# Optimization experiments

Hardware: AMD Instinct MI355X
Metric: run time of the kernel (lower is better)

The kernel has to match this reference:

```python
import jax, jax.numpy as jnp
import numpy as np

N = 8192
H = 256
NF = 256  # number of fragment segments
LOG2 = 0.6931471805599453
R = 0.3        # short_long_ratio
C = 0.8        # brics_consistency_strength
VW = 0.5       # vector_weight


def _ssp(x):
    # ShiftedSoftplus: softplus(x) - log(2)
    return jax.nn.softplus(x) - LOG2


def _l2norm(x):
    # F.normalize(p=2, dim=1) semantics with eps clamp
    n = jnp.linalg.norm(x, axis=1, keepdims=True)
    return x / jnp.maximum(n, 1e-12)


def _pair_sim_err_per_frag(feat, fragment_ids, pair_mask):
    # sum over same-fragment upper-tri pairs of (cos_sim - C)^2, per fragment
    z = _l2norm(feat)                       # [N,H]
    S = z @ z.T                             # [N,N]
    err = jnp.where(pair_mask, (S - C) ** 2, 0.0)
    return jax.ops.segment_sum(err.sum(axis=1), fragment_ids, num_segments=NF)


def setup_inputs() -> dict:
    key = jax.random.key(0)
    ks = jax.random.split(key, 12)
    s = 1.0 / np.sqrt(H)
    return {
        "scalar_short": jax.random.normal(ks[0], (N, H), dtype=jnp.float32),
        "scalar_long": jax.random.normal(ks[1], (N, H), dtype=jnp.float32),
        "vector_short": jax.random.normal(ks[2], (N, 3, H), dtype=jnp.float32),
        "vector_long": jax.random.normal(ks[3], (N, 3, H), dtype=jnp.float32),
        "W1": jax.random.normal(ks[4], (H, H), dtype=jnp.float32) * s,
        "b1": jnp.zeros((H,), dtype=jnp.float32),
        "W2": jax.random.normal(ks[5], (H, H), dtype=jnp.float32) * s,
        "b2": jnp.zeros((H,), dtype=jnp.float32),
        "V1": jax.random.normal(ks[6], (H, H), dtype=jnp.float32) * s,
        "V2": jax.random.normal(ks[7], (H, H), dtype=jnp.float32) * s,
        "fragment_ids": jax.random.randint(ks[8], (N,), 0, NF, dtype=jnp.int64),
    }


def reference(scalar_short, scalar_long, vector_short, vector_long,
              W1, b1, W2, b2, V1, V2, fragment_ids):
    frag = fragment_ids
    counts = jax.ops.segment_sum(jnp.ones((N,), jnp.float32), frag, num_segments=NF)
    n_safe = jnp.maximum(counts, 1.0)
    pair_count = counts * (counts - 1.0) * 0.5
    pc_safe = jnp.maximum(pair_count, 1.0)

    idx = jnp.arange(N)
    # same-fragment, strictly-upper-triangular pair mask [N,N]
    pair_mask = (frag[:, None] == frag[None, :]) & (idx[None, :] > idx[:, None])

    # ---- scalar branch ----
    sc = scalar_short * R + scalar_long * (1.0 - R)
    si = _ssp(sc @ W1 + b1) @ W2 + b2                     # [N,H]
    s_mean = jax.ops.segment_sum(si, frag, num_segments=NF) / n_safe[:, None]
    s_dev = si - s_mean[frag]
    s_var = jax.ops.segment_sum((s_dev ** 2).sum(axis=1), frag, num_segments=NF) / n_safe
    s_sim = _pair_sim_err_per_frag(si, frag, pair_mask) / pc_safe
    scalar_loss = s_var + s_sim

    # ---- vector branch ----
    vc = vector_short * R + vector_long * (1.0 - R)
    vi = _ssp(vc @ V1) @ V2                               # [N,3,H]
    v_mean = jax.ops.segment_sum(vi, frag, num_segments=NF) / n_safe[:, None, None]
    v_dev = vi - v_mean[frag]
    v_var = jax.ops.segment_sum((v_dev ** 2).sum(axis=(1, 2)), frag, num_segments=NF) / n_safe
    dir_err = jnp.zeros((NF,), jnp.float32)
    for d in range(3):
        dir_err = dir_err + _pair_sim_err_per_frag(vi[:, d, :], frag, pair_mask)
    dir_loss = dir_err / (3.0 * pc_safe)
    vector_loss = v_var + dir_loss

    frag_loss = (1.0 - VW) * scalar_loss + VW * vector_loss
    valid = pair_count > 0.0   # fragments with >= 2 nodes
    vcnt = valid.sum().astype(jnp.float32)
    total = jnp.where(valid, frag_loss, 0.0).sum()
    return jnp.where(vcnt > 0.0, total / jnp.maximum(vcnt, 1.0), 0.0)
```

## Files before the change

### kernel.cpp

```cpp
#include <hip/hip_runtime.h>
#include <cmath>

#define N_NODES 8192
#define HDIM 256
#define NFRAG 256
#define RMIX 0.3f
#define CSIM 0.8f
#define LN2 0.6931471805599453f
#define CMAX 64

typedef __bf16 bf16x8 __attribute__((ext_vector_type(8)));
typedef float f32x4 __attribute__((ext_vector_type(4)));
typedef unsigned short us8 __attribute__((ext_vector_type(8)));
typedef unsigned short us4 __attribute__((ext_vector_type(4)));
typedef unsigned short ushort_t;

#define SI_OFF   ((size_t)0)
#define VI_OFF   ((size_t)8388608)
#define WH_OFF   ((size_t)58720256)
#define WL_OFF   ((size_t)59244544)
#define CNT_OFF  ((size_t)59768832)
#define CUR_OFF  (CNT_OFF + 1024)
#define OFF_OFF  (CNT_OFF + 2048)
#define SORT_OFF (CNT_OFF + 3072)
#define ACC_OFF  (SORT_OFF + 32768)
#define FLG_OFF  (ACC_OFF + 128)
#define NRM_OFF  (ACC_OFF + 256)
#define FRGN_OFF (NRM_OFF + 4 * 32768)

__device__ __forceinline__ ushort_t f2bf(float x) {
    unsigned u = __float_as_uint(x);
    return (ushort_t)((u + 0x7FFFu + ((u >> 16) & 1u)) >> 16);
}
__device__ __forceinline__ float bf2f(ushort_t h) {
    return __uint_as_float(((unsigned)h) << 16);
}
__device__ __forceinline__ f32x4 mfma_bf16(us8 a, us8 b, f32x4 c) {
    return __builtin_amdgcn_mfma_f32_16x16x32_bf16(
        __builtin_bit_cast(bf16x8, a), __builtin_bit_cast(bf16x8, b), c, 0, 0, 0);
}


__global__ void init_kernel(int* counts, int* cursor, float* acc, int* flag) {
    int t = threadIdx.x;
    if (t < NFRAG) { counts[t] = 0; cursor[t] = 0; }
    if (t < 8) acc[t] = 0.f;
    if (t == 0) *flag = 0;
}

__global__ void detect_kernel(const int* __restrict__ buf, int* flag) {
    int i = blockIdx.x * 256 + threadIdx.x;
    if (buf[2 * i + 1] != 0) atomicOr(flag, 1);
}

__global__ void normalize_kernel(const int* __restrict__ buf, const int* __restrict__ flag,
                                 int* __restrict__ fragN) {
    int i = blockIdx.x * 256 + threadIdx.x;
    if (i < N_NODES) fragN[i] = (*flag) ? buf[i] : buf[2 * i];
}

__global__ void hist_kernel(const int* __restrict__ frag, int* counts) {
    int i = blockIdx.x * 256 + threadIdx.x;
    if (i < N_NODES) atomicAdd(&counts[frag[i]], 1);
}

__global__ void scan_kernel(const int* __restrict__ counts, int* offs) {
    __shared__ int tmp[NFRAG];
    int t = threadIdx.x;
    tmp[t] = counts[t];
    __syncthreads();
    for (int off = 1; off < NFRAG; off <<= 1) {
        int v = (t >= off) ? tmp[t - off] : 0;
        __syncthreads();
        tmp[t] += v;
        __syncthreads();
    }
    offs[t] = tmp[t] - counts[t];
}

__global__ void scatter_kernel(const int* __restrict__ frag, const int* __restrict__ offs,
                               int* cursor, int* sorted) {
    int i = blockIdx.x * 256 + threadIdx.x;
    if (i < N_NODES) {
        int f = frag[i];
        int pos = offs[f] + atomicAdd(&cursor[f], 1);
        sorted[pos] = i;
    }
}

__global__ void wsplit_kernel(const float* __restrict__ W1, const float* __restrict__ W2,
                              const float* __restrict__ V1, const float* __restrict__ V2,
                              ushort_t* __restrict__ Whi, ushort_t* __restrict__ Wlo) {
    int m = blockIdx.y;
    const float* src = (m == 0) ? W1 : (m == 1) ? W2 : (m == 2) ? V1 : V2;
    ushort_t* dh = Whi + m * 65536;
    ushort_t* dl = Wlo + m * 65536;
    int o = blockIdx.x * 256 + threadIdx.x;
    int e = o & 7, kg = (o >> 3) & 3, n = (o >> 5) & 255, kb = o >> 13;
    float x = src[(size_t)(kb * 32 + kg * 8 + e) * HDIM + n];
    ushort_t h = f2bf(x);
    dh[o] = h;
    dl[o] = f2bf(x - bf2f(h));
}


template<bool BIAS1, bool BIAS2>
__global__ __launch_bounds__(256)
void mlp_fused(const float* __restrict__ A0, const float* __restrict__ A1,
               const ushort_t* __restrict__ B1h, const ushort_t* __restrict__ B1l,
               const ushort_t* __restrict__ B2h, const ushort_t* __restrict__ B2l,
               const float* __restrict__ b1, const float* __restrict__ b2,
               float* __restrict__ Out)
{
    __shared__ ushort_t Zh[32 * 256];
    __shared__ ushort_t Zl[32 * 256];

    const int tid = threadIdx.x;
    const int l   = tid & 63;
    const int wid = tid >> 6;
    const int lr  = l & 15;
    const int kg  = l >> 4;
    const int rowBase = blockIdx.x * 32;
    const int colW = wid * 64;

    {
        int r  = tid >> 3;
        int c0 = (tid & 7) * 32;
        const float* ps = A0 + (size_t)(rowBase + r) * HDIM + c0;
        const float* pl = A1 + (size_t)(rowBase + r) * HDIM + c0;
        int swz = (r & 7) << 3;
        #pragma unroll
        for (int cc = 0; cc < 4; ++cc) {
            float4 s0 = *(const float4*)(ps + cc * 8);
            float4 s1 = *(const float4*)(ps + cc * 8 + 4);
            float4 t0 = *(const float4*)(pl + cc * 8);
            float4 t1 = *(const float4*)(pl + cc * 8 + 4);
            float x[8];
            x[0] = s0.x * RMIX + t0.x * (1.f - RMIX);
            x[1] = s0.y * RMIX + t0.y * (1.f - RMIX);
            x[2] = s0.z * RMIX + t0.z * (1.f - RMIX);
            x[3] = s0.w * RMIX + t0.w * (1.f - RMIX);
            x[4] = s1.x * RMIX + t1.x * (1.f - RMIX);
            x[5] = s1.y * RMIX + t1.y * (1.f - RMIX);
            x[6] = s1.z * RMIX + t1.z * (1.f - RMIX);
            x[7] = s1.w * RMIX + t1.w * (1.f - RMIX);
            us8 h, lo;
            #pragma unroll
            for (int e = 0; e < 8; ++e) {
                ushort_t hh = f2bf(x[e]);
                h[e] = hh;
                lo[e] = f2bf(x[e] - bf2f(hh));
            }
            int idx = r * 256 + ((c0 + cc * 8) ^ swz);
            *(us8*)&Zh[idx] = h;
            *(us8*)&Zl[idx] = lo;
        }
    }
    __syncthreads();

    const ushort_t *w1h[4], *w1l[4], *w2h[4], *w2l[4];
    #pragma unroll
    for (int nf = 0; nf < 4; ++nf) {
        int n = colW + nf * 16 + lr;
        int off = n * 32 + kg * 8;
        w1h[nf] = B1h + off;  w1l[nf] = B1l + off;
        w2h[nf] = B2h + off;  w2l[nf] = B2l + off;
    }

    f32x4 acc[2][4];
    #pragma unroll
    for (int mf = 0; mf < 2; ++mf)
        #pragma unroll
        for (int nf = 0; nf < 4; ++nf)
            acc[mf][nf] = f32x4{0.f, 0.f, 0.f, 0.f};

    for (int kb = 0; kb < 8; ++kb) {
        const int kx = kb * 32 + kg * 8;
        us8 ah[2], al[2];
        #pragma unroll
        for (int mf = 0; mf < 2; ++mf) {
            int m = mf * 16 + lr;
            int idx = m * 256 + (kx ^ ((m & 7) << 3));
            ah[mf] = *(const us8*)&Zh[idx];
            al[mf] = *(const us8*)&Zl[idx];
        }
        #pragma unroll
        for (int nf = 0; nf < 4; ++nf) {
            us8 wh = *(const us8*)(w1h[nf] + kb * 8192);
            us8 wl = *(const us8*)(w1l[nf] + kb * 8192);
            #pragma unroll
            for (int mf = 0; mf < 2; ++mf) {
                f32x4 t = acc[mf][nf];
                t = mfma_bf16(wl, al[mf], t);
                t = mfma_bf16(wl, ah[mf], t);
                t = mfma_bf16(wh, al[mf], t);
                t = mfma_bf16(wh, ah[mf], t);
                acc[mf][nf] = t;
            }
        }
    }
    __syncthreads();

    #pragma unroll
    for (int mf = 0; mf < 2; ++mf) {
        int m = mf * 16 + lr;
        #pragma unroll
        for (int nf = 0; nf < 4; ++nf) {
            int n0 = colW + nf * 16 + kg * 4;
            float4 bb = {0.f, 0.f, 0.f, 0.f};
            if constexpr (BIAS1) bb = *(const float4*)(b1 + n0);
            us4 h4, l4;
            #pragma unroll
            for (int r = 0; r < 4; ++r) {
                float x = acc[mf][nf][r] + ((const float*)&bb)[r];
                x = fmaxf(x, 0.f) + log1pf(__expf(-fabsf(x))) - LN2;
                ushort_t hh = f2bf(x);
                h4[r] = hh;
                l4[r] = f2bf(x - bf2f(hh));
            }
            int idx = m * 256 + (n0 ^ ((m & 7) << 3));
            *(us4*)&Zh[idx] = h4;
            *(us4*)&Zl[idx] = l4;
        }
    }
    __syncthreads();

    f32x4 acc2[2][4];
    #pragma unroll
    for (int mf = 0; mf < 2; ++mf)
        #pragma unroll
        for (int nf = 0; nf < 4; ++nf)
            acc2[mf][nf] = f32x4{0.f, 0.f, 0.f, 0.f};

    for (int kb = 0; kb < 8; ++kb) {
        const int kx = kb * 32 + kg * 8;
        us8 ah[2], al[2];
        #pragma unroll
        for (int mf = 0; mf < 2; ++mf) {
            int m = mf * 16 + lr;
            int idx = m * 256 + (kx ^ ((m & 7) << 3));
            ah[mf] = *(const us8*)&Zh[idx];
            al[mf] = *(const us8*)&Zl[idx];
        }
        #pragma unroll
        for (int nf = 0; nf < 4; ++nf) {
            us8 wh = *(const us8*)(w2h[nf] + kb * 8192);
            us8 wl = *(const us8*)(w2l[nf] + kb * 8192);
            #pragma unroll
            for (int mf = 0; mf < 2; ++mf) {
                f32x4 t = acc2[mf][nf];
                t = mfma_bf16(wl, al[mf], t);
                t = mfma_bf16(wl, ah[mf], t);
                t = mfma_bf16(wh, al[mf], t);
                t = mfma_bf16(wh, ah[mf], t);
                acc2[mf][nf] = t;
            }
        }
    }

    #pragma unroll
    for (int mf = 0; mf < 2; ++mf) {
        int row = rowBase + mf * 16 + lr;
        #pragma unroll
        for (int nf = 0; nf < 4; ++nf) {
            int n0 = colW + nf * 16 + kg * 4;
            float4 bb = {0.f, 0.f, 0.f, 0.f};
            if constexpr (BIAS2) bb = *(const float4*)(b2 + n0);
            float4 v;
            v.x = acc2[mf][nf][0] + bb.x;
            v.y = acc2[mf][nf][1] + bb.y;
            v.z = acc2[mf][nf][2] + bb.z;
            v.w = acc2[mf][nf][3] + bb.w;
            *(float4*)(Out + (size_t)row * HDIM + n0) = v;
        }
    }
}


__device__ __forceinline__ float blockReduceSum(float v, float* red) {
    #pragma unroll
    for (int off = 32; off > 0; off >>= 1)
        v += __shfl_down(v, off, 64);
    __syncthreads();
    if ((threadIdx.x & 63) == 0) red[threadIdx.x >> 6] = v;
    __syncthreads();
    return red[0] + red[1] + red[2] + red[3];
}

__device__ __forceinline__ float dot4(float4 a, float4 b) {
    return a.x * b.x + a.y * b.y + a.z * b.z + a.w * b.w;
}

__device__ void compute_invn_g(const float* __restrict__ Mat, int mult, int doff,
                               int c, int basep, const int* __restrict__ sorted,
                               float* invn, int tid)
{
    for (int p = tid; p < c; p += 256) {
        int nd = sorted[basep + p];
        const float4* row = (const float4*)(Mat + ((size_t)nd * mult + doff) * HDIM);
        float ss = 0.f;
        #pragma unroll 8
        for (int k = 0; k < 64; ++k) {
            float4 v = row[k];
            ss += v.x * v.x + v.y * v.y + v.z * v.z + v.w * v.w;
        }
        invn[p] = 1.0f / fmaxf(sqrtf(ss), 1e-12f);
    }
}

__device__ float pair_err_slow(const float* __restrict__ Mat, int mult, int doff,
                               int c, int basep, const int* __restrict__ sorted,
                               const float* invn, int tid)
{
    float e = 0.f;
    for (long pi = tid; pi < (long)c * c; pi += 256) {
        int i = (int)(pi / c), j = (int)(pi - (long)i * c);
        if (j <= i) continue;
        const float4* ri = (const float4*)(Mat + ((size_t)sorted[basep + i] * mult + doff) * HDIM);
        const float4* rj = (const float4*)(Mat + ((size_t)sorted[basep + j] * mult + doff) * HDIM);
        float dt = 0.f;
        for (int k = 0; k < 64; ++k) dt += dot4(ri[k], rj[k]);
        float sv = dt * invn[i] * invn[j];
        float d = sv - CSIM;
        e += d * d;
    }
    return e;
}

__global__ __launch_bounds__(256)
void fragmat_kernel(const float* __restrict__ SI, const float* __restrict__ VI,
                    const int* __restrict__ counts, const int* __restrict__ offs,
                    const int* __restrict__ sorted, float* acc, float* nrm_global)
{
    const int f = blockIdx.x, m = blockIdx.y, tid = threadIdx.x;
    const int c = counts[f];
    if (c < 2) return;
    const int basep = offs[f];
    const float* Mat = (m == 0) ? SI : VI;
    const int mult = (m == 0) ? 1 : 3;
    const int doff = (m == 0) ? 0 : (m - 1);

    __shared__ __align__(16) float Z[CMAX * 260];
    __shared__ float invn_s[CMAX];
    __shared__ float red[4];

    float var, err;

    if (c <= CMAX) {
        for (int u = tid; u < c * 64; u += 256) {
            int r = u >> 6, kc = u & 63;
            float4 v = *((const float4*)(Mat + ((size_t)sorted[basep + r] * mult + doff) * HDIM) + kc);
            *(float4*)&Z[r * 260 + (kc << 2)] = v;
        }
        __syncthreads();

        float msum = 0.f;
        for (int p = 0; p < c; ++p) msum += Z[p * 260 + tid];
        float mean = msum / (float)c;
        float vh = 0.f;
        for (int p = 0; p < c; ++p) {
            float d = Z[p * 260 + tid] - mean;
            vh += d * d;
        }
        var = blockReduceSum(vh, red);

        for (int p = tid; p < c; p += 256) {
            const float4* row = (const float4*)&Z[p * 260];
            float ss = 0.f;
            #pragma unroll 8
            for (int k = 0; k < 64; ++k) {
                float4 v = row[k];
                ss += v.x * v.x + v.y * v.y + v.z * v.z + v.w * v.w;
            }
            invn_s[p] = 1.0f / fmaxf(sqrtf(ss), 1e-12f);
        }
        __syncthreads();

        const int nb2 = (c + 1) >> 1;
        const int nbp = nb2 * (nb2 + 1) / 2;
        float e = 0.f;
        for (int u = tid; u < nbp; u += 256) {
            int bi = 0, rem = u;
            while (rem >= nb2 - bi) { rem -= nb2 - bi; ++bi; }
            int bj = bi + rem;
            int i0 = bi << 1, j0 = bj << 1;
            const float* zi0 = &Z[i0 * 260];
            const float* zi1 = &Z[(i0 + 1) * 260];
            const float* zj0 = &Z[j0 * 260];
            const float* zj1 = &Z[(j0 + 1) * 260];
            float s00 = 0.f, s01 = 0.f, s10 = 0.f, s11 = 0.f;
            #pragma unroll 4
            for (int k = 0; k < 64; ++k) {
                float4 a0 = *(const float4*)(zi0 + (k << 2));
                float4 a1 = *(const float4*)(zi1 + (k << 2));
                float4 b0 = *(const float4*)(zj0 + (k << 2));
                float4 b1 = *(const float4*)(zj1 + (k << 2));
                s00 += dot4(a0, b0);
                s01 += dot4(a0, b1);
                s10 += dot4(a1, b0);
                s11 += dot4(a1, b1);
            }
            int i1 = i0 + 1, j1 = j0 + 1;
            if (j0 > i0 && j0 < c) { float sv = s00 * invn_s[i0] * invn_s[j0] - CSIM; e += sv * sv; }
            if (j1 > i0 && j1 < c) { float sv = s01 * invn_s[i0] * invn_s[j1] - CSIM; e += sv * sv; }
            if (j0 > i1 && j0 < c) { float sv = s10 * invn_s[i1] * invn_s[j0] - CSIM; e += sv * sv; }
            if (j1 > i1 && j1 < c) { float sv = s11 * invn_s[i1] * invn_s[j1] - CSIM; e += sv * sv; }
        }
        err = blockReduceSum(e, red);
    } else {
        float msum = 0.f;
        for (int p = 0; p < c; ++p)
            msum += Mat[((size_t)sorted[basep + p] * mult + doff) * HDIM + tid];
        float mean = msum / (float)c;
        float vh = 0.f;
        for (int p = 0; p < c; ++p) {
            float d = Mat[((size_t)sorted[basep + p] * mult + doff) * HDIM + tid] - mean;
            vh += d * d;
        }
        var = blockReduceSum(vh, red);

        float* invn = nrm_global + (size_t)m * N_NODES + basep;
        compute_invn_g(Mat, mult, doff, c, basep, sorted, invn, tid);
        __syncthreads();
        float e = pair_err_slow(Mat, mult, doff, c, basep, sorted, invn, tid);
        err = blockReduceSum(e, red);
    }

    if (tid == 0) {
        float n = (float)c;
        float pc = 0.5f * n * (n - 1.f);
        float w_err = (m == 0) ? (0.5f / pc) : (0.5f / (3.f * pc));
        float contrib = 0.5f * var / n + err * w_err;
        atomicAdd(&acc[0], contrib);
        if (m == 0) atomicAdd(&acc[1], 1.0f);
    }
}

__global__ void finalize_kernel(const float* __restrict__ acc, float* __restrict__ out) {
    if (threadIdx.x == 0)
        out[0] = (acc[1] > 0.f) ? acc[0] / acc[1] : 0.f;
}


extern "C" void kernel_launch(void* const* d_in, const int* in_sizes, int n_in,
                              void* d_out, int out_size, void* d_ws, size_t ws_size,
                              hipStream_t stream) {
    const float* s_short = (const float*)d_in[0];
    const float* s_long  = (const float*)d_in[1];
    const float* v_short = (const float*)d_in[2];
    const float* v_long  = (const float*)d_in[3];
    const float* W1 = (const float*)d_in[4];
    const float* b1 = (const float*)d_in[5];
    const float* W2 = (const float*)d_in[6];
    const float* b2 = (const float*)d_in[7];
    const float* V1 = (const float*)d_in[8];
    const float* V2 = (const float*)d_in[9];
    const int* fragRaw = (const int*)d_in[10];
    float* out = (float*)d_out;

    char* ws = (char*)d_ws;
    float*    SI     = (float*)(ws + SI_OFF);
    float*    VI     = (float*)(ws + VI_OFF);
    ushort_t* WH     = (ushort_t*)(ws + WH_OFF);
    ushort_t* WL     = (ushort_t*)(ws + WL_OFF);
    int*      counts = (int*)(ws + CNT_OFF);
    int*      cursor = (int*)(ws + CUR_OFF);
    int*      offs   = (int*)(ws + OFF_OFF);
    int*      sorted = (int*)(ws + SORT_OFF);
    float*    acc    = (float*)(ws + ACC_OFF);
    int*      flag   = (int*)(ws + FLG_OFF);
    float*    nrm    = (float*)(ws + NRM_OFF);
    int*      fragN  = (int*)(ws + FRGN_OFF);

    init_kernel<<<1, 256, 0, stream>>>(counts, cursor, acc, flag);
    detect_kernel<<<16, 256, 0, stream>>>(fragRaw, flag);
    normalize_kernel<<<N_NODES / 256, 256, 0, stream>>>(fragRaw, flag, fragN);
    hist_kernel<<<N_NODES / 256, 256, 0, stream>>>(fragN, counts);
    scan_kernel<<<1, 256, 0, stream>>>(counts, offs);
    scatter_kernel<<<N_NODES / 256, 256, 0, stream>>>(fragN, offs, cursor, sorted);
    wsplit_kernel<<<dim3(256, 4), 256, 0, stream>>>(W1, W2, V1, V2, WH, WL);

    mlp_fused<true, true><<<dim3(N_NODES / 32), 256, 0, stream>>>(
        s_short, s_long, WH + 0 * 65536, WL + 0 * 65536,
        WH + 1 * 65536, WL + 1 * 65536, b1, b2, SI);
    mlp_fused<false, false><<<dim3(3 * N_NODES / 32), 256, 0, stream>>>(
        v_short, v_long, WH + 2 * 65536, WL + 2 * 65536,
        WH + 3 * 65536, WL + 3 * 65536, nullptr, nullptr, VI);

    fragmat_kernel<<<dim3(NFRAG, 4), 256, 0, stream>>>(SI, VI, counts, offs, sorted, acc, nrm);
    finalize_kernel<<<1, 64, 0, stream>>>(acc, out);
}
```

Measured before the change: 255.1 us.

## Merge scalar and vector MLP launches and double row tile to 64

Replaces the two templated MLP launches with one kernel that picks the scalar or vector branch per block from its row index. The block's row tile grows from 32 to 64, so each weight fragment loaded from global memory feeds four M-fragments instead of two, which halves weight traffic per row. The softplus log1pf is also swapped for the faster __logf(1+x). The cost is doubled LDS (64KB) and more accumulator registers, which may lower occupancy, plus a small accuracy change in the softplus.

Measured after the change: 209.5 us. 17.9% less time.

```diff
diff --git a/kernel.cpp b/kernel.cpp
--- a/kernel.cpp
+++ b/kernel.cpp
@@ -104,33 +104,49 @@
 }
 
 
-template<bool BIAS1, bool BIAS2>
 __global__ __launch_bounds__(256)
-void mlp_fused(const float* __restrict__ A0, const float* __restrict__ A1,
-               const ushort_t* __restrict__ B1h, const ushort_t* __restrict__ B1l,
-               const ushort_t* __restrict__ B2h, const ushort_t* __restrict__ B2l,
-               const float* __restrict__ b1, const float* __restrict__ b2,
-               float* __restrict__ Out)
+void mlp_fused_all(const float* __restrict__ s_short, const float* __restrict__ s_long,
+                   const float* __restrict__ v_short, const float* __restrict__ v_long,
+                   const ushort_t* __restrict__ WH, const ushort_t* __restrict__ WL,
+                   const float* __restrict__ b1, const float* __restrict__ b2,
+                   float* __restrict__ SI, float* __restrict__ VI)
 {
-    __shared__ ushort_t Zh[32 * 256];
-    __shared__ ushort_t Zl[32 * 256];
+    __shared__ __align__(16) ushort_t Zh[64 * 256];
+    __shared__ __align__(16) ushort_t Zl[64 * 256];
 
     const int tid = threadIdx.x;
     const int l   = tid & 63;
     const int wid = tid >> 6;
     const int lr  = l & 15;
     const int kg  = l >> 4;
-    const int rowBase = blockIdx.x * 32;
     const int colW = wid * 64;
 
+    const int rowBase = blockIdx.x * 64;
+    const bool isScalar = (rowBase < N_NODES);
+    const float* A0;
+    const float* A1;
+    float* Out;
+    const ushort_t *B1h, *B1l, *B2h, *B2l;
+    if (isScalar) {
+        size_t off = (size_t)rowBase * HDIM;
+        A0 = s_short + off;  A1 = s_long + off;  Out = SI + off;
+        B1h = WH;              B1l = WL;
+        B2h = WH + 65536;      B2l = WL + 65536;
+    } else {
+        size_t off = (size_t)(rowBase - N_NODES) * HDIM;
+        A0 = v_short + off;  A1 = v_long + off;  Out = VI + off;
+        B1h = WH + 2 * 65536;  B1l = WL + 2 * 65536;
+        B2h = WH + 3 * 65536;  B2l = WL + 3 * 65536;
+    }
+
     {
-        int r  = tid >> 3;
-        int c0 = (tid & 7) * 32;
-        const float* ps = A0 + (size_t)(rowBase + r) * HDIM + c0;
-        const float* pl = A1 + (size_t)(rowBase + r) * HDIM + c0;
+        int r  = tid >> 2;
+        int c0 = (tid & 3) * 64;
+        const float* ps = A0 + (size_t)r * HDIM + c0;
+        const float* pl = A1 + (size_t)r * HDIM + c0;
         int swz = (r & 7) << 3;
         #pragma unroll
-        for (int cc = 0; cc < 4; ++cc) {
+        for (int cc = 0; cc < 8; ++cc) {
             float4 s0 = *(const float4*)(ps + cc * 8);
             float4 s1 = *(const float4*)(ps + cc * 8 + 4);
             float4 t0 = *(const float4*)(pl + cc * 8);
@@ -158,62 +174,60 @@
     }
     __syncthreads();
 
-    const ushort_t *w1h[4], *w1l[4], *w2h[4], *w2l[4];
+    const int wbase = (colW + lr) * 32 + kg * 8;
+
+    f32x4 acc[4][4];
     #pragma unroll
-    for (int nf = 0; nf < 4; ++nf) {
-        int n = colW + nf * 16 + lr;
-        int off = n * 32 + kg * 8;
-        w1h[nf] = B1h + off;  w1l[nf] = B1l + off;
-        w2h[nf] = B2h + off;  w2l[nf] = B2l + off;
-    }
-
-    f32x4 acc[2][4];
-    #pragma unroll
-    for (int mf = 0; mf < 2; ++mf)
+    for (int mf = 0; mf < 4; ++mf)
         #pragma unroll
         for (int nf = 0; nf < 4; ++nf)
             acc[mf][nf] = f32x4{0.f, 0.f, 0.f, 0.f};
 
-    for (int kb = 0; kb < 8; ++kb) {
-        const int kx = kb * 32 + kg * 8;
-        us8 ah[2], al[2];
-        #pragma unroll
-        for (int mf = 0; mf < 2; ++mf) {
-            int m = mf * 16 + lr;
-            int idx = m * 256 + (kx ^ ((m & 7) << 3));
-            ah[mf] = *(const us8*)&Zh[idx];
-            al[mf] = *(const us8*)&Zl[idx];
-        }
-        #pragma unroll
-        for (int nf = 0; nf < 4; ++nf) {
-            us8 wh = *(const us8*)(w1h[nf] + kb * 8192);
-            us8 wl = *(const us8*)(w1l[nf] + kb * 8192);
+    {
+        const ushort_t* ph = B1h + wbase;
+        const ushort_t* pl = B1l + wbase;
+        for (int kb = 0; kb < 8; ++kb) {
+            const int kx = kb * 32 + kg * 8;
+            us8 ah[4], al[4];
             #pragma unroll
-            for (int mf = 0; mf < 2; ++mf) {
-                f32x4 t = acc[mf][nf];
-                t = mfma_bf16(wl, al[mf], t);
-                t = mfma_bf16(wl, ah[mf], t);
-                t = mfma_bf16(wh, al[mf], t);
-                t = mfma_bf16(wh, ah[mf], t);
-                acc[mf][nf] = t;
-            }
+            for (int mf = 0; mf < 4; ++mf) {
+                int m = mf * 16 + lr;
+                int idx = m * 256 + (kx ^ ((m & 7) << 3));
+                ah[mf] = *(const us8*)&Zh[idx];
+                al[mf] = *(const us8*)&Zl[idx];
+            }
+            #pragma unroll
+            for (int nf = 0; nf < 4; ++nf) {
+                us8 wh = *(const us8*)(ph + nf * 512);
+                us8 wl = *(const us8*)(pl + nf * 512);
+                #pragma unroll
+                for (int mf = 0; mf < 4; ++mf) {
+                    f32x4 t = acc[mf][nf];
+                    t = mfma_bf16(wl, al[mf], t);
+                    t = mfma_bf16(wl, ah[mf], t);
+                    t = mfma_bf16(wh, al[mf], t);
+                    t = mfma_bf16(wh, ah[mf], t);
+                    acc[mf][nf] = t;
+                }
+            }
+            ph += 8192; pl += 8192;
         }
     }
     __syncthreads();
 
     #pragma unroll
-    for (int mf = 0; mf < 2; ++mf) {
+    for (int mf = 0; mf < 4; ++mf) {
         int m = mf * 16 + lr;
         #pragma unroll
         for (int nf = 0; nf < 4; ++nf) {
             int n0 = colW + nf * 16 + kg * 4;
             float4 bb = {0.f, 0.f, 0.f, 0.f};
-            if constexpr (BIAS1) bb = *(const float4*)(b1 + n0);
+            if (isScalar) bb = *(const float4*)(b1 + n0);
             us4 h4, l4;
             #pragma unroll
             for (int r = 0; r < 4; ++r) {
                 float x = acc[mf][nf][r] + ((const float*)&bb)[r];
-                x = fmaxf(x, 0.f) + log1pf(__expf(-fabsf(x))) - LN2;
+                x = fmaxf(x, 0.f) + __logf(1.f + __expf(-fabsf(x))) - LN2;
                 ushort_t hh = f2bf(x);
                 h4[r] = hh;
                 l4[r] = f2bf(x - bf2f(hh));
@@ -225,53 +239,58 @@
     }
     __syncthreads();
 
-    f32x4 acc2[2][4];
+    f32x4 acc2[4][4];
     #pragma unroll
-    for (int mf = 0; mf < 2; ++mf)
+    for (int mf = 0; mf < 4; ++mf)
         #pragma unroll
         for (int nf = 0; nf < 4; ++nf)
             acc2[mf][nf] = f32x4{0.f, 0.f, 0.f, 0.f};
 
-    for (int kb = 0; kb < 8; ++kb) {
-        const int kx = kb * 32 + kg * 8;
-        us8 ah[2], al[2];
-        #pragma unroll
-        for (int mf = 0; mf < 2; ++mf) {
-            int m = mf * 16 + lr;
-            int idx = m * 256 + (kx ^ ((m & 7) << 3));
-            ah[mf] = *(const us8*)&Zh[idx];
-            al[mf] = *(const us8*)&Zl[idx];
-        }
-        #pragma unroll
-        for (int nf = 0; nf < 4; ++nf) {
-            us8 wh = *(const us8*)(w2h[nf] + kb * 8192);
-            us8 wl = *(const us8*)(w2l[nf] + kb * 8192);
+    {
+        const ushort_t* ph = B2h + wbase;
+        const ushort_t* pl = B2l + wbase;
+        for (int kb = 0; kb < 8; ++kb) {
+            const int kx = kb * 32 + kg * 8;
+            us8 ah[4], al[4];
             #pragma unroll
-            for (int mf = 0; mf < 2; ++mf) {
-                f32x4 t = acc2[mf][nf];
-                t = mfma_bf16(wl, al[mf], t);
-                t = mfma_bf16(wl, ah[mf], t);
-                t = mfma_bf16(wh, al[mf], t);
-                t = mfma_bf16(wh, ah[mf], t);
-                acc2[mf][nf] = t;
-            }
+            for (int mf = 0; mf < 4; ++mf) {
+                int m = mf * 16 + lr;
+                int idx = m * 256 + (kx ^ ((m & 7) << 3));
+                ah[mf] = *(const us8*)&Zh[idx];
+                al[mf] = *(const us8*)&Zl[idx];
+            }
+            #pragma unroll
+            for (int nf = 0; nf < 4; ++nf) {
+                us8 wh = *(const us8*)(ph + nf * 512);
+                us8 wl = *(const us8*)(pl + nf * 512);
+                #pragma unroll
+                for (int mf = 0; mf < 4; ++mf) {
+                    f32x4 t = acc2[mf][nf];
+                    t = mfma_bf16(wl, al[mf], t);
+                    t = mfma_bf16(wl, ah[mf], t);
+                    t = mfma_bf16(wh, al[mf], t);
+                    t = mfma_bf16(wh, ah[mf], t);
+                    acc2[mf][nf] = t;
+                }
+            }
+            ph += 8192; pl += 8192;
         }
     }
 
     #pragma unroll
-    for (int mf = 0; mf < 2; ++mf) {
-        int row = rowBase + mf * 16 + lr;
+    for (int mf = 0; mf < 4; ++mf) {
+        int m = mf * 16 + lr;
         #pragma unroll
         for (int nf = 0; nf < 4; ++nf) {
             int n0 = colW + nf * 16 + kg * 4;
             float4 bb = {0.f, 0.f, 0.f, 0.f};
-            if constexpr (BIAS2) bb = *(const float4*)(b2 + n0);
+            if (isScalar) bb = *(const float4*)(b2 + n0);
             float4 v;
             v.x = acc2[mf][nf][0] + bb.x;
             v.y = acc2[mf][nf][1] + bb.y;
             v.z = acc2[mf][nf][2] + bb.z;
             v.w = acc2[mf][nf][3] + bb.w;
-            *(float4*)(Out + (size_t)row * HDIM + n0) = v;
+            *(float4*)(Out + (size_t)m * HDIM + n0) = v;
         }
     }
 }
@@ -480,12 +499,8 @@
     scatter_kernel<<<N_NODES / 256, 256, 0, stream>>>(fragN, offs, cursor, sorted);
     wsplit_kernel<<<dim3(256, 4), 256, 0, stream>>>(W1, W2, V1, V2, WH, WL);
 
-    mlp_fused<true, true><<<dim3(N_NODES / 32), 256, 0, stream>>>(
-        s_short, s_long, WH + 0 * 65536, WL + 0 * 65536,
-        WH + 1 * 65536, WL + 1 * 65536, b1, b2, SI);
-    mlp_fused<false, false><<<dim3(3 * N_NODES / 32), 256, 0, stream>>>(
-        v_short, v_long, WH + 2 * 65536, WL + 2 * 65536,
-        WH + 3 * 65536, WL + 3 * 65536, nullptr, nullptr, VI);
+    mlp_fused_all<<<dim3((N_NODES + 3 * N_NODES) / 64), 256, 0, stream>>>(
+        s_short, s_long, v_short, v_long, WH, WL, b1, b2, SI, VI);
 
     fragmat_kernel<<<dim3(NFRAG, 4), 256, 0, stream>>>(SI, VI, counts, offs, sorted, acc, nrm);
     finalize_kernel<<<1, 64, 0, stream>>>(acc, out);
```
